# Performance work log

Measured on AMD Instinct MI355X. Metric: run time of the kernel, lower is better.

The kernel has to match this reference:

```python
import jax, jax.numpy as jnp
import numpy as np
import math

B, S, D = 4, 128, 2560
H, HD = 32, 80
FFN = 10240
DEC, ENC = 256, 256
EPS = 1e-5


def setup_inputs() -> dict:
    key = jax.random.key(0)
    ks = iter(jax.random.split(key, 40))

    def w(shape, scale=0.02):
        return jax.random.normal(next(ks), shape, jnp.float32) * scale

    inp = {}
    inp["x"] = jax.random.normal(next(ks), (B, S, D), jnp.float32)
    inp["xa"] = jax.random.normal(next(ks), (B, S, D), jnp.float32)
    # self-attn mask: causal over the S prefill positions, False on unfilled cache tail
    j = jnp.arange(DEC)
    i = jnp.arange(S)
    m = (j[None, :] <= i[:, None]) & (j[None, :] < S)  # [S, DEC]
    inp["mask"] = jnp.broadcast_to(m[None, None], (B, 1, S, DEC))
    inp["cross_mask"] = jnp.broadcast_to((jnp.arange(ENC) < S)[None, None, None], (B, 1, 1, ENC))
    # LayerNorms
    for n in ["ln1", "ln2", "ln3"]:
        inp[n + "_g"] = jnp.ones((D,), jnp.float32)
        inp[n + "_b"] = jnp.zeros((D,), jnp.float32)
    # self-attn projections ([in, out] layout for x @ W)
    for p in ["sa", "ca"]:
        for n in ["wq", "wk", "wv", "wo"]:
            inp[p + "_" + n] = w((D, D))
        for n in ["bq", "bk", "bv", "bo"]:
            inp[p + "_" + n] = jnp.zeros((D,), jnp.float32)
    inp["cache_sk"] = jnp.zeros((B, H, DEC, HD), jnp.float32)
    inp["cache_sv"] = jnp.zeros((B, H, DEC, HD), jnp.float32)
    inp["cache_ck"] = jnp.zeros((B, H, ENC, HD), jnp.float32)
    inp["cache_cv"] = jnp.zeros((B, H, ENC, HD), jnp.float32)
    inp["fc1_w"] = w((D, FFN))
    inp["fc1_b"] = jnp.zeros((FFN,), jnp.float32)
    inp["fc2_w"] = w((FFN, D))
    inp["fc2_b"] = jnp.zeros((D,), jnp.float32)
    return inp


def _ln(h, g, b):
    h32 = h.astype(jnp.float32)
    mu = h32.mean(-1, keepdims=True)
    var = ((h32 - mu) ** 2).mean(-1, keepdims=True)
    return ((h32 - mu) * jax.lax.rsqrt(var + EPS) * g + b).astype(h.dtype)


def _heads(t):
    b, s, _ = t.shape
    return t.reshape(b, s, H, HD).transpose(0, 2, 1, 3)  # [B,H,S,HD]


def _attn(q, k_cache, v_cache, mask):
    kf = k_cache.astype(q.dtype)
    vf = v_cache.astype(q.dtype)
    scores = jnp.einsum("bhqd,bhkd->bhqk", q, kf) / math.sqrt(HD)
    if mask is not None:
        scores = jnp.where(mask, scores, jnp.finfo(scores.dtype).min)
    attn = jax.nn.softmax(scores.astype(jnp.float32), axis=-1).astype(q.dtype)
    o = jnp.einsum("bhqk,bhkd->bhqd", attn, vf)
    b, h, s, hd = o.shape
    return o.transpose(0, 2, 1, 3).reshape(b, s, h * hd)


def reference(x, xa, mask, cross_mask,
              ln1_g, ln1_b, sa_wq, sa_bq, sa_wk, sa_bk, sa_wv, sa_bv, sa_wo, sa_bo,
              cache_sk, cache_sv,
              ln2_g, ln2_b, ca_wq, ca_bq, ca_wk, ca_bk, ca_wv, ca_bv, ca_wo, ca_bo,
              cache_ck, cache_cv,
              ln3_g, ln3_b, fc1_w, fc1_b, fc2_w, fc2_b):
    # --- self-attention (prefill path: scatter with arange indices = prefix write) ---
    h = _ln(x, ln1_g, ln1_b)
    q = _heads(h @ sa_wq + sa_bq)
    k = _heads(h @ sa_wk + sa_bk)
    v = _heads(h @ sa_wv + sa_bv)
    s = q.shape[2]
    sk = cache_sk.at[:, :, :s, :].set(k.astype(jnp.float32))
    sv = cache_sv.at[:, :, :s, :].set(v.astype(jnp.float32))
    o = _attn(q, sk, sv, mask)
    x = x + (o @ sa_wo + sa_bo)

    # --- cross-attention: K/V from encoder output, scattered into cache ---
    h = _ln(x, ln2_g, ln2_b)
    q = _heads(h @ ca_wq + ca_bq)
    k = _heads(xa @ ca_wk + ca_bk)
    v = _heads(xa @ ca_wv + ca_bv)
    kv = k.shape[2]
    ck = cache_ck.at[:, :, :kv, :].set(k.astype(jnp.float32))
    cv = cache_cv.at[:, :, :kv, :].set(v.astype(jnp.float32))
    o = _attn(q, ck, cv, cross_mask)
    x = x + (o @ ca_wo + ca_bo)

    # --- MLP: fc1 -> GELU (exact) -> fc2 ---
    h = _ln(x, ln3_g, ln3_b)
    x = x + (jax.nn.gelu(h @ fc1_w + fc1_b, approximate=False) @ fc2_w + fc2_b)
    return (x, sk, sv, ck, cv)
```

## Files before the change

kernel.cpp:

```cpp
#include <hip/hip_runtime.h>
#include <hip/hip_bf16.h>
#include <math.h>

#define TB   4
#define TS   128
#define TD   2560
#define TH   32
#define THD  80
#define TFFN 10240
#define TDEC 256
#define TM   (TB * TS)
#define CACHE_N ((size_t)TB * TH * TDEC * THD)

using short8  = __attribute__((ext_vector_type(8))) short;
using sshort4 = __attribute__((ext_vector_type(4))) short;
using floatx4 = __attribute__((ext_vector_type(4))) float;

__device__ __forceinline__ short f2bf(float f) {
  unsigned u = __builtin_bit_cast(unsigned, f);
  u += 0x7fff + ((u >> 16) & 1);
  return (short)(u >> 16);
}
__device__ __forceinline__ float bf2f(short s) {
  unsigned u = ((unsigned)(unsigned short)s) << 16;
  return __builtin_bit_cast(float, u);
}

struct GArgs {
  const short* A[3];
  const float* B[3];
  float*       outf[3];
  int tilesPerSeg;
  int N;
  int lda;
  int Kc;
};

__device__ __forceinline__ void stage_load(const short* __restrict__ A,
                                           const float* __restrict__ B,
                                           int lda, int N, int m0, int n0, int k0,
                                           int tid, short8 ra[2], float rb[16])
{
  const int cb = (tid & 3) * 8;
  const int rr = tid >> 2;
#pragma unroll
  for (int it = 0; it < 2; ++it)
    ra[it] = *(const short8*)(A + (size_t)(m0 + rr + it * 64) * lda + k0 + cb);
  const int n  = tid & 127;
  const int kg = (tid >> 7) * 16;
  const float* bp = B + (size_t)(k0 + kg) * N + n0 + n;
#pragma unroll
  for (int j = 0; j < 16; ++j)
    rb[j] = bp[(size_t)j * N];
}

__device__ __forceinline__ void stage_commit(short* __restrict__ As, short* __restrict__ Bs,
                                             int tid, const short8 ra[2], const float rb[16])
{
  const int cb = (tid & 3) * 8;
  const int rr = tid >> 2;
#pragma unroll
  for (int it = 0; it < 2; ++it)
    *(short8*)(&As[(rr + it * 64) * 40 + cb]) = ra[it];
  const int n  = tid & 127;
  const int kg = (tid >> 7) * 16;
  short8 lo, hi;
#pragma unroll
  for (int j = 0; j < 8; ++j) { lo[j] = f2bf(rb[j]); hi[j] = f2bf(rb[8 + j]); }
  *(short8*)(&Bs[n * 40 + kg])     = lo;
  *(short8*)(&Bs[n * 40 + kg + 8]) = hi;
}

__global__ __launch_bounds__(256, 2)
void gemmF(GArgs g)
{
  __shared__ short As[2][128 * 40];
  __shared__ short Bs[2][128 * 40];

  const int seg = blockIdx.x / g.tilesPerSeg;
  const int tx  = blockIdx.x % g.tilesPerSeg;
  const short* A = g.A[seg];
  const float* B = g.B[seg];
  const int N = g.N, lda = g.lda;
  const int m0 = blockIdx.y * 128;
  const int n0 = tx * 128;
  const int z  = blockIdx.z;
  const int k0base = z * g.Kc;
  const int nk = g.Kc / 32;

  const int tid = threadIdx.x;
  const int lane = tid & 63;
  const int wv = tid >> 6;
  const int wm = (wv >> 1) * 64;
  const int wn = (wv & 1) * 64;
  const int lr = lane & 15;
  const int lq = lane >> 4;

  floatx4 acc[4][4];
#pragma unroll
  for (int i = 0; i < 4; ++i)
#pragma unroll
    for (int j = 0; j < 4; ++j)
      acc[i][j] = floatx4{0.f, 0.f, 0.f, 0.f};

  short8 ra[2]; float rb[16];
  stage_load(A, B, lda, N, m0, n0, k0base, tid, ra, rb);
  stage_commit(As[0], Bs[0], tid, ra, rb);
  __syncthreads();

  for (int ki = 0; ki < nk; ++ki) {
    const int cur = ki & 1;
    const bool more = (ki + 1 < nk);
    if (more)
      stage_load(A, B, lda, N, m0, n0, k0base + (ki + 1) * 32, tid, ra, rb);

    short8 af[4], bfr[4];
#pragma unroll
    for (int t = 0; t < 4; ++t)
      af[t] = *(const short8*)(&As[cur][(wm + t * 16 + lr) * 40 + lq * 8]);
#pragma unroll
    for (int t = 0; t < 4; ++t)
      bfr[t] = *(const short8*)(&Bs[cur][(wn + t * 16 + lr) * 40 + lq * 8]);
#pragma unroll
    for (int tm = 0; tm < 4; ++tm)
#pragma unroll
      for (int tn = 0; tn < 4; ++tn)
        acc[tm][tn] = __builtin_amdgcn_mfma_f32_16x16x32_bf16(af[tm], bfr[tn],
                                                              acc[tm][tn], 0, 0, 0);
    if (more)
      stage_commit(As[cur ^ 1], Bs[cur ^ 1], tid, ra, rb);
    __syncthreads();
  }

  float* outf = g.outf[seg];
#pragma unroll
  for (int tm = 0; tm < 4; ++tm) {
#pragma unroll
    for (int tn = 0; tn < 4; ++tn) {
      const int col = n0 + wn + tn * 16 + lr;
#pragma unroll
      for (int r = 0; r < 4; ++r) {
        const int row = m0 + wm + tm * 16 + lq * 4 + r;
        outf[(size_t)z * TM * N + (size_t)row * N + col] = acc[tm][tn][r];
      }
    }
  }
}

template<int Z>
__global__ void qkv_combine_kernel(const float* __restrict__ p,
                                   const float* __restrict__ bq,
                                   const float* __restrict__ bk,
                                   const float* __restrict__ bv,
                                   float* __restrict__ qbuf,
                                   float* __restrict__ sk,
                                   float* __restrict__ sv)
{
  const int i4 = blockIdx.x * 256 + threadIdx.x;
  const int row = i4 / 1920;
  const int c4  = i4 - row * 1920;
  const int col = c4 * 4;
  const int seg = (col >= 2 * TD) ? 2 : (col >= TD ? 1 : 0);
  const int c   = col - seg * TD;
  const float* base = p + (size_t)seg * ((size_t)Z * TM * TD) + (size_t)row * TD + c;
  float4 v = *(const float4*)base;
#pragma unroll
  for (int zz = 1; zz < Z; ++zz) {
    float4 t = *(const float4*)(base + (size_t)zz * TM * TD);
    v.x += t.x; v.y += t.y; v.z += t.z; v.w += t.w;
  }
  const float* bias = (seg == 0) ? bq : (seg == 1 ? bk : bv);
  float4 b4 = *(const float4*)(bias + c);
  v.x += b4.x; v.y += b4.y; v.z += b4.z; v.w += b4.w;
  if (seg == 0) {
    *(float4*)(qbuf + (size_t)row * TD + c) = v;
  } else {
    const int hh = c / THD, hd = c % THD;
    const int b = row >> 7, sI = row & 127;
    float* dst = (seg == 1) ? sk : sv;
    *(float4*)(dst + (((size_t)(b * TH + hh) * TDEC + sI) * THD + hd)) = v;
  }
}

template<int Z>
__global__ void fc1_gelu_kernel(const float* __restrict__ p,
                                const float* __restrict__ bias,
                                short* __restrict__ out)
{
  const int i4 = blockIdx.x * 256 + threadIdx.x;
  const int row = i4 / (TFFN / 4);
  const int c4  = i4 - row * (TFFN / 4);
  const int col = c4 * 4;
  const size_t idx = (size_t)row * TFFN + col;
  float4 v = *(const float4*)(p + idx);
#pragma unroll
  for (int zz = 1; zz < Z; ++zz) {
    float4 t = *(const float4*)(p + (size_t)zz * TM * TFFN + idx);
    v.x += t.x; v.y += t.y; v.z += t.z; v.w += t.w;
  }
  float4 b4 = *(const float4*)(bias + col);
  v.x += b4.x; v.y += b4.y; v.z += b4.z; v.w += b4.w;
  sshort4 o;
  o[0] = f2bf(0.5f * v.x * (1.0f + erff(v.x * 0.70710678118654752f)));
  o[1] = f2bf(0.5f * v.y * (1.0f + erff(v.y * 0.70710678118654752f)));
  o[2] = f2bf(0.5f * v.z * (1.0f + erff(v.z * 0.70710678118654752f)));
  o[3] = f2bf(0.5f * v.w * (1.0f + erff(v.w * 0.70710678118654752f)));
  *(sshort4*)(out + idx) = o;
}

template<bool CAUSAL>
__global__ __launch_bounds__(256, 2)
void attn_kernel(const float* __restrict__ q, const float* __restrict__ kc,
                 const float* __restrict__ vc, short* __restrict__ ob)
{
  __shared__ short kb[TS * THD];
  __shared__ short vb[TS * THD];
  __shared__ float qf[64 * 84];
  short* pb = (short*)qf;

  const int tid = threadIdx.x;
  const int bh = blockIdx.x;
  const int b = bh >> 5, h = bh & 31;
  const int r0 = blockIdx.y * 64;

  const size_t cbase = (size_t)bh * TDEC * THD;
  for (int idx = tid; idx < TS * THD; idx += 256) {
    kb[idx] = f2bf(kc[cbase + idx]);
    vb[idx] = f2bf(vc[cbase + idx]);
  }
  for (int idx = tid; idx < 64 * THD; idx += 256) {
    int r = idx / THD, d = idx - r * THD;
    qf[r * 84 + d] = q[(size_t)(b * TS + r0 + r) * TD + h * THD + d];
  }
  __syncthreads();

  const int r = tid >> 2;
  const int quarter = tid & 3;
  const int qi = r0 + r;

  float sc[32];
#pragma unroll 1
  for (int jj = 0; jj < 32; ++jj) {
    int j = quarter + jj * 4;
    if (CAUSAL && j > qi) { sc[jj] = -1e30f; continue; }
    float a = 0.f;
#pragma unroll 8
    for (int d = 0; d < THD; ++d)
      a += qf[r * 84 + d] * bf2f(kb[j * THD + d]);
    sc[jj] = a * 0.11180339887498949f;
  }

  float mx = -1e30f;
#pragma unroll
  for (int jj = 0; jj < 32; ++jj) mx = fmaxf(mx, sc[jj]);
  mx = fmaxf(mx, __shfl_xor(mx, 1));
  mx = fmaxf(mx, __shfl_xor(mx, 2));
  float sum = 0.f;
#pragma unroll
  for (int jj = 0; jj < 32; ++jj) { sc[jj] = __expf(sc[jj] - mx); sum += sc[jj]; }
  sum += __shfl_xor(sum, 1);
  sum += __shfl_xor(sum, 2);
  const float rinv = 1.0f / sum;

  __syncthreads();
#pragma unroll
  for (int jj = 0; jj < 32; ++jj)
    pb[r * TS + quarter + jj * 4] = f2bf(sc[jj] * rinv);
  __syncthreads();

  for (int it = 0; it < 20; ++it) {
    int idx = tid + it * 256;
    int rr = idx / THD, d = idx - rr * THD;
    float a = 0.f;
#pragma unroll 8
    for (int j = 0; j < TS; ++j)
      a += bf2f(pb[rr * TS + j]) * bf2f(vb[j * THD + d]);
    ob[(size_t)(b * TS + r0 + rr) * TD + h * THD + d] = f2bf(a);
  }
}

__global__ __launch_bounds__(256, 4)
void ln_kernel(const float* __restrict__ x, const float* __restrict__ g,
               const float* __restrict__ bb, short* __restrict__ out)
{
  const int row = blockIdx.x;
  const float* xr = x + (size_t)row * TD;
  const int tid = threadIdx.x;
  float vals[10];
  float s = 0.f, ss = 0.f;
#pragma unroll
  for (int it = 0; it < 10; ++it) {
    float v = xr[tid + it * 256];
    vals[it] = v; s += v; ss += v * v;
  }
#pragma unroll
  for (int o = 32; o > 0; o >>= 1) { s += __shfl_xor(s, o); ss += __shfl_xor(ss, o); }
  __shared__ float red[8];
  const int wv = tid >> 6, lane = tid & 63;
  if (lane == 0) { red[wv] = s; red[wv + 4] = ss; }
  __syncthreads();
  s  = red[0] + red[1] + red[2] + red[3];
  ss = red[4] + red[5] + red[6] + red[7];
  const float mu = s * (1.0f / TD);
  const float rstd = rsqrtf(ss * (1.0f / TD) - mu * mu + 1e-5f);
  short* orow = out + (size_t)row * TD;
#pragma unroll
  for (int it = 0; it < 10; ++it) {
    int i = tid + it * 256;
    orow[i] = f2bf((vals[it] - mu) * rstd * g[i] + bb[i]);
  }
}

template<int Z>
__global__ __launch_bounds__(256, 4)
void ln_fuse_kernel(const float* __restrict__ xin, const float* __restrict__ p,
                    const float* __restrict__ obias,
                    const float* __restrict__ g, const float* __restrict__ bb,
                    short* __restrict__ hout, float* __restrict__ xout)
{
  const int row = blockIdx.x;
  const int tid = threadIdx.x;
  const size_t base = (size_t)row * TD;
  float vals[10];
  float s = 0.f, ss = 0.f;
#pragma unroll
  for (int it = 0; it < 10; ++it) {
    int i = tid + it * 256;
    float v = xin[base + i] + obias[i];
#pragma unroll
    for (int zz = 0; zz < Z; ++zz)
      v += p[(size_t)zz * TM * TD + base + i];
    vals[it] = v; xout[base + i] = v; s += v; ss += v * v;
  }
#pragma unroll
  for (int o = 32; o > 0; o >>= 1) { s += __shfl_xor(s, o); ss += __shfl_xor(ss, o); }
  __shared__ float red[8];
  const int wv = tid >> 6, lane = tid & 63;
  if (lane == 0) { red[wv] = s; red[wv + 4] = ss; }
  __syncthreads();
  s  = red[0] + red[1] + red[2] + red[3];
  ss = red[4] + red[5] + red[6] + red[7];
  const float mu = s * (1.0f / TD);
  const float rstd = rsqrtf(ss * (1.0f / TD) - mu * mu + 1e-5f);
#pragma unroll
  for (int it = 0; it < 10; ++it) {
    int i = tid + it * 256;
    hout[base + i] = f2bf((vals[it] - mu) * rstd * g[i] + bb[i]);
  }
}

template<int Z>
__global__ void fc2_combine_kernel(const float* __restrict__ x2, const float* __restrict__ p,
                                   const float* __restrict__ bias, float* __restrict__ out)
{
  const size_t i = ((size_t)blockIdx.x * 256 + threadIdx.x) * 4;
  const int col = (int)(i % TD);
  float4 v = *(const float4*)(x2 + i);
#pragma unroll
  for (int zz = 0; zz < Z; ++zz) {
    float4 t = *(const float4*)(p + (size_t)zz * TM * TD + i);
    v.x += t.x; v.y += t.y; v.z += t.z; v.w += t.w;
  }
  float4 b4 = *(const float4*)(bias + col);
  v.x += b4.x; v.y += b4.y; v.z += b4.z; v.w += b4.w;
  *(float4*)(out + i) = v;
}

__global__ void cvt_bf16_kernel(const float* __restrict__ in, short* __restrict__ out, int n)
{
  int i = blockIdx.x * 256 + threadIdx.x;
  if (i < n) out[i] = f2bf(in[i]);
}

__global__ void tailcopy_kernel(const float* __restrict__ src, float* __restrict__ dst)
{
  int off4 = blockIdx.x * 256 + threadIdx.x;
  int chunk = blockIdx.y;
  size_t pos = (size_t)chunk * 5120 + 2560 + off4;
  ((float4*)dst)[pos] = ((const float4*)src)[pos];
}

extern "C" void kernel_launch(void* const* d_in, const int* in_sizes, int n_in,
                              void* d_out, int out_size, void* d_ws, size_t ws_size,
                              hipStream_t stream)
{
  (void)in_sizes; (void)n_in; (void)out_size; (void)ws_size;
  const float* x        = (const float*)d_in[0];
  const float* xa       = (const float*)d_in[1];
  const float* ln1_g    = (const float*)d_in[4];
  const float* ln1_b    = (const float*)d_in[5];
  const float* ln2_g    = (const float*)d_in[6];
  const float* ln2_b    = (const float*)d_in[7];
  const float* ln3_g    = (const float*)d_in[8];
  const float* ln3_b    = (const float*)d_in[9];
  const float* sa_wq    = (const float*)d_in[10];
  const float* sa_wk    = (const float*)d_in[11];
  const float* sa_wv    = (const float*)d_in[12];
  const float* sa_wo    = (const float*)d_in[13];
  const float* sa_bq    = (const float*)d_in[14];
  const float* sa_bk    = (const float*)d_in[15];
  const float* sa_bv    = (const float*)d_in[16];
  const float* sa_bo    = (const float*)d_in[17];
  const float* ca_wq    = (const float*)d_in[18];
  const float* ca_wk    = (const float*)d_in[19];
  const float* ca_wv    = (const float*)d_in[20];
  const float* ca_wo    = (const float*)d_in[21];
  const float* ca_bq    = (const float*)d_in[22];
  const float* ca_bk    = (const float*)d_in[23];
  const float* ca_bv    = (const float*)d_in[24];
  const float* ca_bo    = (const float*)d_in[25];
  const float* cache_sk = (const float*)d_in[26];
  const float* cache_sv = (const float*)d_in[27];
  const float* cache_ck = (const float*)d_in[28];
  const float* cache_cv = (const float*)d_in[29];
  const float* fc1_w    = (const float*)d_in[30];
  const float* fc1_b    = (const float*)d_in[31];
  const float* fc2_w    = (const float*)d_in[32];
  const float* fc2_b    = (const float*)d_in[33];

  float* out_x  = (float*)d_out;
  float* out_sk = out_x + (size_t)TM * TD;
  float* out_sv = out_sk + CACHE_N;
  float* out_ck = out_sv + CACHE_N;
  float* out_cv = out_ck + CACHE_N;

  char* w = (char*)d_ws;
  short* h_b   = (short*)w; w += (size_t)TM * TD * 2;
  short* xa_b  = (short*)w; w += (size_t)TM * TD * 2;
  short* o_b   = (short*)w; w += (size_t)TM * TD * 2;
  short* ffn_b = (short*)w; w += (size_t)TM * TFFN * 2;
  float* qbuf  = (float*)w; w += (size_t)TM * TD * 4;
  float* x1    = (float*)w; w += (size_t)TM * TD * 4;
  float* x2    = (float*)w; w += (size_t)TM * TD * 4;
  float* pbuf  = (float*)w; w += (size_t)TM * TD * 4 * 12;

  const dim3 blk(256);
  const dim3 gAttn(TB * TH, 2);

  cvt_bf16_kernel<<<dim3(TM * TD / 256), blk, 0, stream>>>(xa, xa_b, TM * TD);
  tailcopy_kernel<<<dim3(10, TB * TH), blk, 0, stream>>>(cache_sk, out_sk);
  tailcopy_kernel<<<dim3(10, TB * TH), blk, 0, stream>>>(cache_sv, out_sv);
  tailcopy_kernel<<<dim3(10, TB * TH), blk, 0, stream>>>(cache_ck, out_ck);
  tailcopy_kernel<<<dim3(10, TB * TH), blk, 0, stream>>>(cache_cv, out_cv);

  ln_kernel<<<dim3(TM), blk, 0, stream>>>(x, ln1_g, ln1_b, h_b);
  {
    GArgs a{};
    a.A[0] = h_b; a.B[0] = sa_wq; a.outf[0] = pbuf;
    a.A[1] = h_b; a.B[1] = sa_wk; a.outf[1] = pbuf + (size_t)4 * TM * TD;
    a.A[2] = h_b; a.B[2] = sa_wv; a.outf[2] = pbuf + (size_t)8 * TM * TD;
    a.tilesPerSeg = 20; a.N = TD; a.lda = TD; a.Kc = TD / 4;
    gemmF<<<dim3(60, 4, 4), blk, 0, stream>>>(a);
  }
  qkv_combine_kernel<4><<<dim3(TM * 7680 / 4 / 256), blk, 0, stream>>>(
      pbuf, sa_bq, sa_bk, sa_bv, qbuf, out_sk, out_sv);
  attn_kernel<true><<<gAttn, blk, 0, stream>>>(qbuf, out_sk, out_sv, o_b);
  {
    GArgs a{};
    a.A[0] = o_b; a.B[0] = sa_wo; a.outf[0] = pbuf;
    a.tilesPerSeg = 20; a.N = TD; a.lda = TD; a.Kc = TD / 8;
    gemmF<<<dim3(20, 4, 8), blk, 0, stream>>>(a);
  }
  ln_fuse_kernel<8><<<dim3(TM), blk, 0, stream>>>(x, pbuf, sa_bo, ln2_g, ln2_b, h_b, x1);

  {
    GArgs a{};
    a.A[0] = h_b;  a.B[0] = ca_wq; a.outf[0] = pbuf;
    a.A[1] = xa_b; a.B[1] = ca_wk; a.outf[1] = pbuf + (size_t)4 * TM * TD;
    a.A[2] = xa_b; a.B[2] = ca_wv; a.outf[2] = pbuf + (size_t)8 * TM * TD;
    a.tilesPerSeg = 20; a.N = TD; a.lda = TD; a.Kc = TD / 4;
    gemmF<<<dim3(60, 4, 4), blk, 0, stream>>>(a);
  }
  qkv_combine_kernel<4><<<dim3(TM * 7680 / 4 / 256), blk, 0, stream>>>(
      pbuf, ca_bq, ca_bk, ca_bv, qbuf, out_ck, out_cv);
  attn_kernel<false><<<gAttn, blk, 0, stream>>>(qbuf, out_ck, out_cv, o_b);
  {
    GArgs a{};
    a.A[0] = o_b; a.B[0] = ca_wo; a.outf[0] = pbuf;
    a.tilesPerSeg = 20; a.N = TD; a.lda = TD; a.Kc = TD / 8;
    gemmF<<<dim3(20, 4, 8), blk, 0, stream>>>(a);
  }
  ln_fuse_kernel<8><<<dim3(TM), blk, 0, stream>>>(x1, pbuf, ca_bo, ln3_g, ln3_b, h_b, x2);

  {
    GArgs a{};
    a.A[0] = h_b; a.B[0] = fc1_w; a.outf[0] = pbuf;
    a.tilesPerSeg = 80; a.N = TFFN; a.lda = TD; a.Kc = TD / 2;
    gemmF<<<dim3(80, 4, 2), blk, 0, stream>>>(a);
  }
  fc1_gelu_kernel<2><<<dim3(TM * TFFN / 4 / 256), blk, 0, stream>>>(pbuf, fc1_b, ffn_b);
  {
    GArgs a{};
    a.A[0] = ffn_b; a.B[0] = fc2_w; a.outf[0] = pbuf;
    a.tilesPerSeg = 20; a.N = TD; a.lda = TFFN; a.Kc = TFFN / 8;
    gemmF<<<dim3(20, 4, 8), blk, 0, stream>>>(a);
  }
  fc2_combine_kernel<8><<<dim3(TM * TD / 4 / 256), blk, 0, stream>>>(x2, pbuf, fc2_b, out_x);
}
```

Measured before the change: 893.1 us.

## Single-buffer LDS GEMM with two-deep register prefetch and grouped block swizzle

Replaces the double-buffered shared-memory GEMM with one LDS buffer plus two register prefetch stages, cutting LDS use so launch bounds can request three blocks per CU. The 3D grid is flattened to 1D and swizzled so that groups of 8 N-tiles run across all 4 M-tiles together, aiming for better L2 reuse of the fp32 weight tiles. In exchange, each k-step now needs two barriers because the single buffer must be drained before it is rewritten, which serializes compute and the LDS commit.

```diff
diff --git a/kernel.cpp b/kernel.cpp
--- a/kernel.cpp
+++ b/kernel.cpp
@@ -31,6 +31,7 @@
   const float* B[3];
   float*       outf[3];
   int tilesPerSeg;
+  int nx;
   int N;
   int lda;
   int Kc;
@@ -71,20 +72,45 @@
   *(short8*)(&Bs[n * 40 + kg + 8]) = hi;
 }
 
-__global__ __launch_bounds__(256, 2)
+__device__ __forceinline__ void compute_step(const short* __restrict__ As,
+                                             const short* __restrict__ Bs,
+                                             int wm, int wn, int lr, int lq,
+                                             floatx4 acc[4][4])
+{
+  short8 af[4], bfr[4];
+#pragma unroll
+  for (int t = 0; t < 4; ++t)
+    af[t] = *(const short8*)(&As[(wm + t * 16 + lr) * 40 + lq * 8]);
+#pragma unroll
+  for (int t = 0; t < 4; ++t)
+    bfr[t] = *(const short8*)(&Bs[(wn + t * 16 + lr) * 40 + lq * 8]);
+#pragma unroll
+  for (int tm = 0; tm < 4; ++tm)
+#pragma unroll
+    for (int tn = 0; tn < 4; ++tn)
+      acc[tm][tn] = __builtin_amdgcn_mfma_f32_16x16x32_bf16(af[tm], bfr[tn],
+                                                            acc[tm][tn], 0, 0, 0);
+}
+
+__global__ __launch_bounds__(256, 3)
 void gemmF(GArgs g)
 {
-  __shared__ short As[2][128 * 40];
-  __shared__ short Bs[2][128 * 40];
-
-  const int seg = blockIdx.x / g.tilesPerSeg;
-  const int tx  = blockIdx.x % g.tilesPerSeg;
+  __shared__ short As[128 * 40];
+  __shared__ short Bs[128 * 40];
+
+  const int raw = blockIdx.x;
+  const int grp = ((raw >> 5) << 3) | (raw & 7);
+  const int my  = (raw >> 3) & 3;
+  const int z   = grp / g.nx;
+  const int x   = grp - z * g.nx;
+  const int seg = x / g.tilesPerSeg;
+  const int tx  = x - seg * g.tilesPerSeg;
+
   const short* A = g.A[seg];
   const float* B = g.B[seg];
   const int N = g.N, lda = g.lda;
-  const int m0 = blockIdx.y * 128;
+  const int m0 = my * 128;
   const int n0 = tx * 128;
-  const int z  = blockIdx.z;
   const int k0base = z * g.Kc;
   const int nk = g.Kc / 32;
 
@@ -103,33 +129,30 @@
     for (int j = 0; j < 4; ++j)
       acc[i][j] = floatx4{0.f, 0.f, 0.f, 0.f};
 
-  short8 ra[2]; float rb[16];
-  stage_load(A, B, lda, N, m0, n0, k0base, tid, ra, rb);
-  stage_commit(As[0], Bs[0], tid, ra, rb);
+  short8 raP[2], raF[2];
+  float  rbP[16], rbF[16];
+
+  stage_load(A, B, lda, N, m0, n0, k0base, tid, raP, rbP);
+  stage_commit(As, Bs, tid, raP, rbP);
   __syncthreads();
-
-  for (int ki = 0; ki < nk; ++ki) {
-    const int cur = ki & 1;
-    const bool more = (ki + 1 < nk);
-    if (more)
-      stage_load(A, B, lda, N, m0, n0, k0base + (ki + 1) * 32, tid, ra, rb);
-
-    short8 af[4], bfr[4];
-#pragma unroll
-    for (int t = 0; t < 4; ++t)
-      af[t] = *(const short8*)(&As[cur][(wm + t * 16 + lr) * 40 + lq * 8]);
-#pragma unroll
-    for (int t = 0; t < 4; ++t)
-      bfr[t] = *(const short8*)(&Bs[cur][(wn + t * 16 + lr) * 40 + lq * 8]);
-#pragma unroll
-    for (int tm = 0; tm < 4; ++tm)
-#pragma unroll
-      for (int tn = 0; tn < 4; ++tn)
-        acc[tm][tn] = __builtin_amdgcn_mfma_f32_16x16x32_bf16(af[tm], bfr[tn],
-                                                              acc[tm][tn], 0, 0, 0);
-    if (more)
-      stage_commit(As[cur ^ 1], Bs[cur ^ 1], tid, ra, rb);
+  stage_load(A, B, lda, N, m0, n0, k0base + 32, tid, raP, rbP);
+
+  for (int ki = 0; ki < nk; ki += 2) {
+    if (ki + 2 < nk)
+      stage_load(A, B, lda, N, m0, n0, k0base + (ki + 2) * 32, tid, raF, rbF);
+    compute_step(As, Bs, wm, wn, lr, lq, acc);
     __syncthreads();
+    stage_commit(As, Bs, tid, raP, rbP);
+    __syncthreads();
+
+    if (ki + 3 < nk)
+      stage_load(A, B, lda, N, m0, n0, k0base + (ki + 3) * 32, tid, raP, rbP);
+    compute_step(As, Bs, wm, wn, lr, lq, acc);
+    if (ki + 2 < nk) {
+      __syncthreads();
+      stage_commit(As, Bs, tid, raF, rbF);
+      __syncthreads();
+    }
   }
 
   float* outf = g.outf[seg];
@@ -449,8 +472,8 @@
     a.A[0] = h_b; a.B[0] = sa_wq; a.outf[0] = pbuf;
     a.A[1] = h_b; a.B[1] = sa_wk; a.outf[1] = pbuf + (size_t)4 * TM * TD;
     a.A[2] = h_b; a.B[2] = sa_wv; a.outf[2] = pbuf + (size_t)8 * TM * TD;
-    a.tilesPerSeg = 20; a.N = TD; a.lda = TD; a.Kc = TD / 4;
-    gemmF<<<dim3(60, 4, 4), blk, 0, stream>>>(a);
+    a.tilesPerSeg = 20; a.nx = 60; a.N = TD; a.lda = TD; a.Kc = TD / 4;
+    gemmF<<<dim3(960), blk, 0, stream>>>(a);
   }
   qkv_combine_kernel<4><<<dim3(TM * 7680 / 4 / 256), blk, 0, stream>>>(
       pbuf, sa_bq, sa_bk, sa_bv, qbuf, out_sk, out_sv);
@@ -458,8 +481,8 @@
   {
     GArgs a{};
     a.A[0] = o_b; a.B[0] = sa_wo; a.outf[0] = pbuf;
-    a.tilesPerSeg = 20; a.N = TD; a.lda = TD; a.Kc = TD / 8;
-    gemmF<<<dim3(20, 4, 8), blk, 0, stream>>>(a);
+    a.tilesPerSeg = 20; a.nx = 20; a.N = TD; a.lda = TD; a.Kc = TD / 8;
+    gemmF<<<dim3(640), blk, 0, stream>>>(a);
   }
   ln_fuse_kernel<8><<<dim3(TM), blk, 0, stream>>>(x, pbuf, sa_bo, ln2_g, ln2_b, h_b, x1);
 
@@ -468,8 +491,8 @@
     a.A[0] = h_b;  a.B[0] = ca_wq; a.outf[0] = pbuf;
     a.A[1] = xa_b; a.B[1] = ca_wk; a.outf[1] = pbuf + (size_t)4 * TM * TD;
     a.A[2] = xa_b; a.B[2] = ca_wv; a.outf[2] = pbuf + (size_t)8 * TM * TD;
-    a.tilesPerSeg = 20; a.N = TD; a.lda = TD; a.Kc = TD / 4;
-    gemmF<<<dim3(60, 4, 4), blk, 0, stream>>>(a);
+    a.tilesPerSeg = 20; a.nx = 60; a.N = TD; a.lda = TD; a.Kc = TD / 4;
+    gemmF<<<dim3(960), blk, 0, stream>>>(a);
   }
   qkv_combine_kernel<4><<<dim3(TM * 7680 / 4 / 256), blk, 0, stream>>>(
       pbuf, ca_bq, ca_bk, ca_bv, qbuf, out_ck, out_cv);
@@ -477,23 +500,23 @@
   {
     GArgs a{};
     a.A[0] = o_b; a.B[0] = ca_wo; a.outf[0] = pbuf;
-    a.tilesPerSeg = 20; a.N = TD; a.lda = TD; a.Kc = TD / 8;
-    gemmF<<<dim3(20, 4, 8), blk, 0, stream>>>(a);
+    a.tilesPerSeg = 20; a.nx = 20; a.N = TD; a.lda = TD; a.Kc = TD / 8;
+    gemmF<<<dim3(640), blk, 0, stream>>>(a);
   }
   ln_fuse_kernel<8><<<dim3(TM), blk, 0, stream>>>(x1, pbuf, ca_bo, ln3_g, ln3_b, h_b, x2);
 
   {
     GArgs a{};
     a.A[0] = h_b; a.B[0] = fc1_w; a.outf[0] = pbuf;
-    a.tilesPerSeg = 80; a.N = TFFN; a.lda = TD; a.Kc = TD / 2;
-    gemmF<<<dim3(80, 4, 2), blk, 0, stream>>>(a);
+    a.tilesPerSeg = 80; a.nx = 80; a.N = TFFN; a.lda = TD; a.Kc = TD / 2;
+    gemmF<<<dim3(640), blk, 0, stream>>>(a);
   }
   fc1_gelu_kernel<2><<<dim3(TM * TFFN / 4 / 256), blk, 0, stream>>>(pbuf, fc1_b, ffn_b);
   {
     GArgs a{};
     a.A[0] = ffn_b; a.B[0] = fc2_w; a.outf[0] = pbuf;
-    a.tilesPerSeg = 20; a.N = TD; a.lda = TFFN; a.Kc = TFFN / 8;
-    gemmF<<<dim3(20, 4, 8), blk, 0, stream>>>(a);
+    a.tilesPerSeg = 20; a.nx = 20; a.N = TD; a.lda = TFFN; a.Kc = TFFN / 8;
+    gemmF<<<dim3(640), blk, 0, stream>>>(a);
   }
   fc2_combine_kernel<8><<<dim3(TM * TD / 4 / 256), blk, 0, stream>>>(x2, pbuf, fc2_b, out_x);
 }
```

Result: no change. 888.1 us (-0.6%).
